# Kernel optimization log

Measured on AMD Instinct MI355X. Metric: run time of the kernel, lower is better.

## Reference

```python
import jax, jax.numpy as jnp
import numpy as np

B, LT, LI, D, H, K = 32, 512, 576, 768, 8, 512


def setup_inputs() -> dict:
    key = jax.random.key(0)
    ks = jax.random.split(key, 10)
    s = 0.02
    return {
        "text_hidden_states": jax.random.normal(ks[0], (B, LT, D), jnp.float32),
        "image_hidden_states": jax.random.normal(ks[1], (B, LI, D), jnp.float32),
        "text_mask": jnp.ones((B, LT), jnp.int32),
        "Wb": jax.random.normal(ks[2], (H, D, D), jnp.float32) * s,   # per-head Linear weights [out,in]
        "Wv": jax.random.normal(ks[3], (K, D), jnp.float32) * s,
        "Wq": jax.random.normal(ks[4], (K, D), jnp.float32) * s,
        "Whv": jax.random.normal(ks[5], (K,), jnp.float32) * s,
        "Whq": jax.random.normal(ks[6], (K,), jnp.float32) * s,
        "Wo": jax.random.normal(ks[7], (D, D * H), jnp.float32) * s,  # output_proj weight [out,in]
        "bo": jnp.zeros((D,), jnp.float32),
    }


def reference(text_hidden_states, image_hidden_states, text_mask, Wb, Wv, Wq, Whv, Whq, Wo, bo):
    text, image = text_hidden_states, image_hidden_states
    # per-head text projection (torch Linear: x @ W.T), batched over heads
    pt = jnp.einsum('bxe,hfe->hbxf', text, Wb)                 # [H,B,LT,D]
    aff = jnp.einsum('hbxe,bye->hbxy', pt, image)              # [H,B,LT,LI]
    wv_v = jnp.einsum('bye,ke->byk', image, Wv)                # [B,LI,K] (head-shared)
    wq_q = jnp.einsum('bxe,ke->bxk', text, Wq)                 # [B,LT,K]
    wqqc = jnp.einsum('bxk,hbxy->hbyk', wq_q, aff)             # [H,B,LI,K]
    wvvc = jnp.einsum('byk,hbxy->hbxk', wv_v, aff)             # [H,B,LT,K]
    h_v = jnp.tanh(wv_v[None] + wqqc)
    h_q = jnp.tanh(wq_q[None] + wvvc)
    att_v = jax.nn.softmax(jnp.einsum('hbyk,k->hby', h_v, Whv), axis=-1)  # over image tokens
    att_q = jax.nn.softmax(jnp.einsum('hbxk,k->hbx', h_q, Whq), axis=-1)  # over text tokens
    ctx_v = jnp.einsum('hby,byd->hbd', att_v, image)
    ctx_q = jnp.einsum('hbx,bxd->hbd', att_q, text)
    head_out = ctx_v + ctx_q                                   # [H,B,D]
    combined = jnp.transpose(head_out, (1, 0, 2)).reshape(text.shape[0], -1)  # [B,H*D]
    return combined @ Wo.T + bo
```

## Files before the change

kernel.cpp:

```cpp
#include <hip/hip_runtime.h>
#include <math.h>

#define B_  32
#define LT_ 512
#define LI_ 576
#define LIP 640
#define D_  768
#define H_  8
#define K_  512
#define NTOK  (LI_ + LT_)
#define CSPLIT 8
#define TPB   (NTOK / CSPLIT)
#define NHEAD ((long)H_ * B_ * D_)

typedef __attribute__((ext_vector_type(4))) short short4v;
typedef __attribute__((ext_vector_type(8))) unsigned short ushort8;
typedef __attribute__((ext_vector_type(8))) _Float16 f16x8;
typedef __attribute__((ext_vector_type(4))) float f32x4;

__device__ __forceinline__ unsigned short f2h(float x) {
  _Float16 h = (_Float16)x;
  return __builtin_bit_cast(unsigned short, h);
}
__device__ __forceinline__ float h2f(unsigned short u) {
  return (float)__builtin_bit_cast(_Float16, u);
}
__device__ __forceinline__ float ftanh(float x) {
  float e = __expf(2.f * x);
  return 1.f - 2.f * __builtin_amdgcn_rcpf(e + 1.f);
}

__device__ __forceinline__ void gl_lds16(const void* g, void* l) {
  __builtin_amdgcn_global_load_lds(
      (const __attribute__((address_space(1))) void*)g,
      (__attribute__((address_space(3))) void*)l, 16, 0, 0);
}

__device__ __forceinline__ f16x8 lds_read16(const unsigned short* p) {
  f16x8 r;
  const __attribute__((address_space(3))) unsigned short* lp =
      (const __attribute__((address_space(3))) unsigned short*)p;
  asm volatile("ds_read_b128 %0, %1" : "=v"(r) : "v"(lp));
  return r;
}

#define EPI_PLAIN 0
#define EPI_T     1
#define EPI_TANH  2
#define EPI_OUT   3

struct Seg {
  const unsigned short *A, *B;
  unsigned short *C, *CT;
  const unsigned short* base;
  const float* wvec;
  float* outv;
  long sA, sB, sC, sCT, sBase;
  int Kd, lda, ldb;
  int gx, gy, nblk, epi, Mlim, valid, ldc, ldt;
};
struct Params { Seg s0, s1, s2; };

__global__ __launch_bounds__(512, 6) void mfma_seg(Params p)
{
  const int orig = blockIdx.x, nwg = gridDim.x;
  const int q8 = nwg >> 3, r8 = nwg & 7;
  const int xcd = orig & 7, idx = orig >> 3;
  const int wg = (xcd < r8 ? xcd * (q8 + 1) : r8 * (q8 + 1) + (xcd - r8) * q8) + idx;

  Seg sg; int local;
  if (wg < p.s0.nblk)                      { sg = p.s0; local = wg; }
  else if (wg < p.s0.nblk + p.s1.nblk)     { sg = p.s1; local = wg - p.s0.nblk; }
  else                                     { sg = p.s2; local = wg - p.s0.nblk - p.s1.nblk; }

  const int bx = local % sg.gx;
  const int tmp2 = local / sg.gx;
  const int by = tmp2 % sg.gy, bz = tmp2 / sg.gy;

  __shared__ unsigned short LDSU[24576];

  const int t = threadIdx.x, lane = t & 63, w = t >> 6;
  const int wr = w >> 2, wc = w & 3;
  const int m0 = bx * 128, n0 = by * 128;
  const int Kd = sg.Kd, lda = sg.lda, ldb = sg.ldb, ldc = sg.ldc;
  const unsigned short* A  = sg.A + (long)bz * sg.sA;
  const unsigned short* Bm = sg.B + (long)bz * sg.sB;

  const int srow = w * 16 + (lane >> 2);
  const int cswz = ((lane & 3) ^ ((srow >> 1) & 3)) * 8;
  const bool clampA = (m0 + 128 > sg.Mlim);
  const unsigned short* aSrc = A  + (long)(m0 + srow) * lda + cswz;
  const unsigned short* bSrc = Bm + (long)(n0 + srow) * ldb + cswz;
  const int ldsLane = w * 512 + lane * 8;

  f32x4 acc[4][2];
  #pragma unroll
  for (int i = 0; i < 4; ++i)
    #pragma unroll
    for (int j = 0; j < 2; ++j)
      acc[i][j] = (f32x4){0.f, 0.f, 0.f, 0.f};

  const int rl = lane & 15, g = lane >> 4;
  const int aslot = (g ^ ((rl >> 1) & 3)) << 3;

  auto stage = [&](int bufi, int k0) {
    unsigned short* Ab = LDSU + bufi * 8192;
    unsigned short* Bb = Ab + 4096;
    if (!clampA) {
      gl_lds16(aSrc + k0, Ab + ldsLane);
    } else {
      int r0 = m0 + srow;
      if (r0 >= sg.Mlim) r0 = sg.Mlim - 1;
      gl_lds16(A + (long)r0 * lda + cswz + k0, Ab + ldsLane);
    }
    gl_lds16(bSrc + k0, Bb + ldsLane);
  };

  const int nt = Kd >> 5;
  stage(0, 0); stage(1, 32); stage(2, 64);
  for (int tt = 0; tt < nt; ++tt) {
    const int ahead = nt - 1 - tt;
    if (ahead >= 2)      asm volatile("s_waitcnt vmcnt(4)" ::: "memory");
    else if (ahead == 1) asm volatile("s_waitcnt vmcnt(2)" ::: "memory");
    else                 asm volatile("s_waitcnt vmcnt(0)" ::: "memory");
    __builtin_amdgcn_s_barrier();

    const unsigned short* Ab = LDSU + (tt % 3) * 8192;
    const unsigned short* Bb = Ab + 4096;
    f16x8 af[4], bf[2];
    #pragma unroll
    for (int i = 0; i < 4; ++i)
      af[i] = lds_read16(&Ab[(wr * 64 + i * 16 + rl) * 32 + aslot]);
    #pragma unroll
    for (int j = 0; j < 2; ++j)
      bf[j] = lds_read16(&Bb[(wc * 32 + j * 16 + rl) * 32 + aslot]);
    asm volatile("s_waitcnt lgkmcnt(0)" ::: "memory");
    __builtin_amdgcn_sched_barrier(0);

    __builtin_amdgcn_s_setprio(1);
    #pragma unroll
    for (int i = 0; i < 4; ++i)
      #pragma unroll
      for (int j = 0; j < 2; ++j)
        acc[i][j] = __builtin_amdgcn_mfma_f32_16x16x32_f16(af[i], bf[j], acc[i][j], 0, 0, 0);
    __builtin_amdgcn_s_setprio(0);

    __builtin_amdgcn_s_barrier();
    if (tt + 3 < nt) stage(tt % 3, (tt + 3) << 5);
  }

  const int rg = lane >> 4;
  if (sg.epi <= EPI_T) {
    unsigned short* C = sg.C + (long)bz * sg.sC;
    unsigned short hv[4][2][4];
    #pragma unroll
    for (int i = 0; i < 4; ++i)
      #pragma unroll
      for (int j = 0; j < 2; ++j)
        #pragma unroll
        for (int rr = 0; rr < 4; ++rr) {
          int ml = wr * 64 + i * 16 + rg * 4 + rr;
          int nl = wc * 32 + j * 16 + rl;
          hv[i][j][rr] = f2h(acc[i][j][rr]);
          if (m0 + ml < sg.Mlim)
            C[(long)(m0 + ml) * ldc + n0 + nl] = hv[i][j][rr];
        }
    if (sg.epi == EPI_T) {
      unsigned short* CT = sg.CT + (long)bz * sg.sCT;
      #pragma unroll
      for (int i = 0; i < 4; ++i)
        #pragma unroll
        for (int j = 0; j < 2; ++j) {
          int nl = wc * 32 + j * 16 + rl;
          int mh = wr * 64 + i * 16 + rg * 4;
          *(short4v*)&LDSU[nl * 136 + mh] = (short4v){
              (short)hv[i][j][0], (short)hv[i][j][1],
              (short)hv[i][j][2], (short)hv[i][j][3]};
        }
      __syncthreads();
      #pragma unroll
      for (int rr = 0; rr < 4; ++rr) {
        int rn = rr * 32 + (t >> 4);
        int m8 = (t & 15) * 8;
        if (m0 + m8 < sg.Mlim)
          *(ushort8*)(CT + (long)(n0 + rn) * sg.ldt + m0 + m8) =
              *(const ushort8*)&LDSU[rn * 136 + m8];
      }
    }
  } else if (sg.epi == EPI_TANH) {
    const unsigned short* base = sg.base + (long)bz * sg.sBase;
    float* outp = sg.outv + (long)bz * sg.valid;
    #pragma unroll
    for (int i = 0; i < 4; ++i)
      #pragma unroll
      for (int rr = 0; rr < 4; ++rr) {
        int row = m0 + wr * 64 + i * 16 + rg * 4 + rr;
        if (row < sg.Mlim) {
          float s = 0.f;
          #pragma unroll
          for (int j = 0; j < 2; ++j) {
            int col = n0 + wc * 32 + j * 16 + rl;
            float v = acc[i][j][rr] + h2f(base[(long)row * ldc + col]);
            s += ftanh(v) * sg.wvec[col];
          }
          s += __shfl_xor(s, 1, 64);
          s += __shfl_xor(s, 2, 64);
          s += __shfl_xor(s, 4, 64);
          s += __shfl_xor(s, 8, 64);
          if (rl == 0 && row < sg.valid)
            atomicAdd(&outp[row], s);
        }
      }
  } else {
    float* outp = sg.outv;
    if (wr == 0) {
      #pragma unroll
      for (int i = 0; i < 2; ++i)
        #pragma unroll
        for (int rr = 0; rr < 4; ++rr) {
          int row = i * 16 + rg * 4 + rr;
          #pragma unroll
          for (int j = 0; j < 2; ++j) {
            int col = n0 + wc * 32 + j * 16 + rl;
            atomicAdd(&outp[(long)row * ldc + col], acc[i][j][rr]);
          }
        }
    }
  }
}

struct CSeg { const float* src; unsigned short* dst; long n8; };

__global__ __launch_bounds__(256) void cast_multi(
    CSeg c0, CSeg c1, CSeg c2, CSeg c3, CSeg c4)
{
  long i = (long)blockIdx.x * 256 + threadIdx.x;
  const float* src; unsigned short* dst;
  if      (i < c0.n8)                 { src = c0.src; dst = c0.dst; }
  else if ((i -= c0.n8) < c1.n8)      { src = c1.src; dst = c1.dst; }
  else if ((i -= c1.n8) < c2.n8)      { src = c2.src; dst = c2.dst; }
  else if ((i -= c2.n8) < c3.n8)      { src = c3.src; dst = c3.dst; }
  else if ((i -= c3.n8) < c4.n8)      { src = c4.src; dst = c4.dst; }
  else return;
  float4 v0 = ((const float4*)src)[i * 2];
  float4 v1 = ((const float4*)src)[i * 2 + 1];
  ushort8 o;
  o[0] = f2h(v0.x); o[1] = f2h(v0.y); o[2] = f2h(v0.z); o[3] = f2h(v0.w);
  o[4] = f2h(v1.x); o[5] = f2h(v1.y); o[6] = f2h(v1.z); o[7] = f2h(v1.w);
  *(ushort8*)(dst + i * 8) = o;
}

__global__ __launch_bounds__(256) void cast_pad_image(
    const float* __restrict__ in, unsigned short* __restrict__ out)
{
  long tid = (long)blockIdx.x * 256 + threadIdx.x;
  const long tot = (long)B_ * LIP * (D_ / 8);
  if (tid >= tot) return;
  int e8 = (int)(tid % (D_ / 8));
  long rw = tid / (D_ / 8);
  int y  = (int)(rw % LIP);
  long b = rw / LIP;
  ushort8 o;
  if (y < LI_) {
    const float* p = in + ((b * LI_ + y) * D_ + e8 * 8);
    float4 v0 = *(const float4*)p, v1 = *(const float4*)(p + 4);
    o[0] = f2h(v0.x); o[1] = f2h(v0.y); o[2] = f2h(v0.z); o[3] = f2h(v0.w);
    o[4] = f2h(v1.x); o[5] = f2h(v1.y); o[6] = f2h(v1.z); o[7] = f2h(v1.w);
  } else {
    #pragma unroll
    for (int j = 0; j < 8; ++j) o[j] = 0;
  }
  *(ushort8*)(out + rw * D_ + e8 * 8) = o;
}

__global__ __launch_bounds__(256) void zero_f32(float* __restrict__ p, long n) {
  long i = (long)blockIdx.x * 256 + threadIdx.x;
  if (i < n) p[i] = 0.f;
}

__global__ __launch_bounds__(256) void init_out(
    const float* __restrict__ bo, float* __restrict__ out)
{
  int i = blockIdx.x * 256 + threadIdx.x;
  out[i] = bo[i % D_];
}

__global__ __launch_bounds__(256) void softmax_att(
    const float* __restrict__ lv, const float* __restrict__ lq,
    float* __restrict__ attvG, float* __restrict__ attqG)
{
  const int b = blockIdx.x, h = blockIdx.y;
  const int t = threadIdx.x;
  __shared__ float buf[LI_];
  __shared__ float red[4];

  const float* lvp = lv + ((long)h * B_ + b) * LI_;
  float m = -1e30f;
  for (int i = t; i < LI_; i += 256) m = fmaxf(m, lvp[i]);
  #pragma unroll
  for (int o = 32; o > 0; o >>= 1) m = fmaxf(m, __shfl_down(m, o, 64));
  if ((t & 63) == 0) red[t >> 6] = m;
  __syncthreads();
  m = fmaxf(fmaxf(red[0], red[1]), fmaxf(red[2], red[3]));
  __syncthreads();
  float s = 0.f;
  for (int i = t; i < LI_; i += 256) { float e = __expf(lvp[i] - m); buf[i] = e; s += e; }
  #pragma unroll
  for (int o = 32; o > 0; o >>= 1) s += __shfl_down(s, o, 64);
  if ((t & 63) == 0) red[t >> 6] = s;
  __syncthreads();
  s = red[0] + red[1] + red[2] + red[3];
  {
    float inv = 1.f / s;
    float* op = attvG + ((long)h * B_ + b) * LI_;
    for (int i = t; i < LI_; i += 256) op[i] = buf[i] * inv;
  }
  __syncthreads();

  const float* lqp = lq + ((long)h * B_ + b) * LT_;
  m = -1e30f;
  for (int i = t; i < LT_; i += 256) m = fmaxf(m, lqp[i]);
  #pragma unroll
  for (int o = 32; o > 0; o >>= 1) m = fmaxf(m, __shfl_down(m, o, 64));
  if ((t & 63) == 0) red[t >> 6] = m;
  __syncthreads();
  m = fmaxf(fmaxf(red[0], red[1]), fmaxf(red[2], red[3]));
  __syncthreads();
  s = 0.f;
  for (int i = t; i < LT_; i += 256) { float e = __expf(lqp[i] - m); buf[i] = e; s += e; }
  #pragma unroll
  for (int o = 32; o > 0; o >>= 1) s += __shfl_down(s, o, 64);
  if ((t & 63) == 0) red[t >> 6] = s;
  __syncthreads();
  s = red[0] + red[1] + red[2] + red[3];
  {
    float inv = 1.f / s;
    float* op = attqG + ((long)h * B_ + b) * LT_;
    for (int i = t; i < LT_; i += 256) op[i] = buf[i] * inv;
  }
}

__global__ __launch_bounds__(256) void ctx_part(
    const float* __restrict__ attvG, const float* __restrict__ attqG,
    const unsigned short* __restrict__ text_h,
    float* __restrict__ head_part)
{
  const int b = blockIdx.x, d0 = blockIdx.y * 128, s = blockIdx.z;
  const int t = threadIdx.x, dl = t & 127, g = t >> 7;
  const long IMG_OFF = (long)B_ * LT_ * D_;
  __shared__ float wts[H_][TPB];
  __shared__ long  roff[TPB];
  __shared__ float red[H_][128];
  const int tok0 = s * TPB;
  for (int i = t; i < H_ * TPB; i += 256) {
    int h = i / TPB, j = i % TPB, tok = tok0 + j;
    wts[h][j] = tok < LI_ ? attvG[((long)h * B_ + b) * LI_ + tok]
                          : attqG[((long)h * B_ + b) * LT_ + (tok - LI_)];
  }
  if (t < TPB) {
    int tok = tok0 + t;
    roff[t] = tok < LI_ ? IMG_OFF + ((long)b * LIP + tok) * D_
                        : ((long)b * LT_ + (tok - LI_)) * D_;
  }
  __syncthreads();
  float acc[H_];
  #pragma unroll
  for (int h = 0; h < H_; ++h) acc[h] = 0.f;
  #pragma unroll 4
  for (int j = g; j < TPB; j += 2) {
    float val = h2f(text_h[roff[j] + d0 + dl]);
    #pragma unroll
    for (int h = 0; h < H_; ++h) acc[h] = fmaf(wts[h][j], val, acc[h]);
  }
  if (g == 1) {
    #pragma unroll
    for (int h = 0; h < H_; ++h) red[h][dl] = acc[h];
  }
  __syncthreads();
  if (g == 0) {
    float* hp = head_part + (long)s * NHEAD;
    #pragma unroll
    for (int h = 0; h < H_; ++h)
      hp[((long)h * B_ + b) * D_ + d0 + dl] = acc[h] + red[h][dl];
  }
}

__global__ __launch_bounds__(256) void reduce_head(
    const float* __restrict__ head_part, unsigned short* __restrict__ head16)
{
  long i = (long)blockIdx.x * 256 + threadIdx.x;
  float s = 0.f;
  #pragma unroll
  for (int p = 0; p < CSPLIT; ++p) s += head_part[(long)p * NHEAD + i];
  int d = (int)(i % D_);
  long hb = i / D_;
  int b = (int)(hb % B_), h = (int)(hb / B_);
  head16[(long)b * (H_ * D_) + (long)h * D_ + d] = f2h(s);
}

extern "C" void kernel_launch(void* const* d_in, const int* in_sizes, int n_in,
                              void* d_out, int out_size, void* d_ws, size_t ws_size,
                              hipStream_t stream)
{
  const float* text  = (const float*)d_in[0];
  const float* image = (const float*)d_in[1];
  const float* Wb  = (const float*)d_in[3];
  const float* Wv  = (const float*)d_in[4];
  const float* Wq  = (const float*)d_in[5];
  const float* Whv = (const float*)d_in[6];
  const float* Whq = (const float*)d_in[7];
  const float* Wo  = (const float*)d_in[8];
  const float* bo  = (const float*)d_in[9];
  float* out = (float*)d_out;

  const long N_TEXT = (long)B_ * LT_ * D_;
  const long N_IMGP = (long)B_ * LIP * D_;
  const long N_WV   = (long)K_ * D_;
  const long N_WB   = (long)H_ * D_ * D_;
  const long N_WO   = (long)D_ * H_ * D_;
  const long N_WVV  = (long)B_ * LIP * K_;
  const long N_WQQ  = (long)B_ * LT_ * K_;
  const long N_PT   = (long)B_ * LT_ * D_;
  const long N_AFF  = (long)B_ * LT_ * LIP;
  const long N_LV   = (long)H_ * B_ * LI_;
  const long N_LQ   = (long)H_ * B_ * LT_;
  const long N_H16  = (long)B_ * H_ * D_;

  unsigned short* wsu = (unsigned short*)d_ws;
  long off = 0;
  unsigned short* text_h  = wsu + off; off += N_TEXT;
  unsigned short* image_p = wsu + off; off += N_IMGP;
  unsigned short* Wv_h    = wsu + off; off += N_WV;
  unsigned short* Wq_h    = wsu + off; off += N_WV;
  unsigned short* Wb_h    = wsu + off; off += N_WB;
  unsigned short* Wo_h    = wsu + off; off += N_WO;
  unsigned short* wv_v    = wsu + off; off += N_WVV;
  unsigned short* wq_q    = wsu + off; off += N_WQQ;
  unsigned short* wv_vT   = wsu + off; off += N_WVV;
  unsigned short* wq_qT   = wsu + off; off += N_WQQ;
  unsigned short* pt_h    = wsu + off; off += N_PT;
  unsigned short* aff     = wsu + off; off += N_AFF;
  unsigned short* affT    = wsu + off; off += N_AFF;
  unsigned short* head16  = wsu + off; off += N_H16;
  float* lv        = (float*)(wsu + off);
  float* lq        = lv + N_LV;
  float* attvG     = lq + N_LQ;
  float* attqG     = attvG + N_LV;
  float* head_part = attqG + N_LQ;
  const size_t need = (size_t)off * 2 +
      (size_t)(2 * (N_LV + N_LQ) + CSPLIT * NHEAD) * 4;
  if (ws_size < need) return;

  dim3 blk(256);
  dim3 blkG(512);

  {
    CSeg c0{text, text_h, N_TEXT / 8};
    CSeg c1{Wv,   Wv_h,   N_WV / 8};
    CSeg c2{Wq,   Wq_h,   N_WV / 8};
    CSeg c3{Wb,   Wb_h,   N_WB / 8};
    CSeg c4{Wo,   Wo_h,   N_WO / 8};
    long tot8 = c0.n8 + c1.n8 + c2.n8 + c3.n8 + c4.n8;
    cast_multi<<<(unsigned)((tot8 + 255) / 256), blk, 0, stream>>>(c0, c1, c2, c3, c4);
  }
  cast_pad_image<<<(unsigned)((B_ * LIP * (D_ / 8) + 255) / 256), blk, 0, stream>>>(image, image_p);
  zero_f32<<<(unsigned)((N_LV + N_LQ + 255) / 256), blk, 0, stream>>>(lv, N_LV + N_LQ);
  init_out<<<(unsigned)(B_ * D_ / 256), blk, 0, stream>>>(bo, out);

  Seg zs{};  zs.nblk = 0;

  {
    Seg s0{}; s0.A = image_p; s0.B = Wv_h; s0.C = wv_v; s0.CT = wv_vT;
    s0.sA = (long)LIP * D_; s0.sC = (long)LIP * K_; s0.sCT = (long)K_ * LIP;
    s0.Kd = D_; s0.lda = D_; s0.ldb = D_;
    s0.gx = 5; s0.gy = 4; s0.nblk = 5 * 4 * B_; s0.epi = EPI_T;
    s0.Mlim = LIP; s0.ldc = K_; s0.ldt = LIP;

    Seg s1{}; s1.A = text_h; s1.B = Wq_h; s1.C = wq_q; s1.CT = wq_qT;
    s1.sA = (long)LT_ * D_; s1.sC = (long)LT_ * K_; s1.sCT = (long)K_ * LT_;
    s1.Kd = D_; s1.lda = D_; s1.ldb = D_;
    s1.gx = 4; s1.gy = 4; s1.nblk = 4 * 4 * B_; s1.epi = EPI_T;
    s1.Mlim = LT_; s1.ldc = K_; s1.ldt = LT_;

    Seg s2{}; s2.A = text_h; s2.B = Wb_h; s2.C = pt_h;
    s2.Kd = D_; s2.lda = D_; s2.ldb = D_;
    s2.gx = 128; s2.gy = 6; s2.nblk = 128 * 6; s2.epi = EPI_PLAIN;
    s2.Mlim = B_ * LT_; s2.ldc = D_;

    Params P{s0, s1, s2};
    mfma_seg<<<s0.nblk + s1.nblk + s2.nblk, blkG, 0, stream>>>(P);
  }

  for (int h = 0; h < H_; ++h) {
    {
      Seg s0{}; s0.A = pt_h; s0.B = image_p; s0.C = aff; s0.CT = affT;
      s0.sA = (long)LT_ * D_; s0.sB = (long)LIP * D_;
      s0.sC = (long)LT_ * LIP; s0.sCT = (long)LIP * LT_;
      s0.Kd = D_; s0.lda = D_; s0.ldb = D_;
      s0.gx = 4; s0.gy = 5; s0.nblk = 4 * 5 * B_; s0.epi = EPI_T;
      s0.Mlim = LT_; s0.ldc = LIP; s0.ldt = LT_;
      Params P{s0, zs, zs};
      mfma_seg<<<s0.nblk, blkG, 0, stream>>>(P);
    }
    {
      Seg s0{}; s0.A = affT; s0.B = wq_qT;
      s0.base = wv_v; s0.wvec = Whv; s0.outv = lv + (long)h * B_ * LI_;
      s0.sA = (long)LIP * LT_; s0.sB = (long)K_ * LT_; s0.sBase = (long)LIP * K_;
      s0.Kd = LT_; s0.lda = LT_; s0.ldb = LT_;
      s0.gx = 5; s0.gy = 4; s0.nblk = 5 * 4 * B_; s0.epi = EPI_TANH;
      s0.Mlim = LIP; s0.valid = LI_; s0.ldc = K_;

      Seg s1{}; s1.A = aff; s1.B = wv_vT;
      s1.base = wq_q; s1.wvec = Whq; s1.outv = lq + (long)h * B_ * LT_;
      s1.sA = (long)LT_ * LIP; s1.sB = (long)K_ * LIP; s1.sBase = (long)LT_ * K_;
      s1.Kd = LIP; s1.lda = LIP; s1.ldb = LIP;
      s1.gx = 4; s1.gy = 4; s1.nblk = 4 * 4 * B_; s1.epi = EPI_TANH;
      s1.Mlim = LT_; s1.valid = LT_; s1.ldc = K_;

      Seg s2 = zs;
      if (h < H_ - 1) {
        s2.A = text_h; s2.B = Wb_h + (long)(h + 1) * D_ * D_; s2.C = pt_h;
        s2.Kd = D_; s2.lda = D_; s2.ldb = D_;
        s2.gx = 128; s2.gy = 6; s2.nblk = 128 * 6; s2.epi = EPI_PLAIN;
        s2.Mlim = B_ * LT_; s2.ldc = D_;
      }
      Params P{s0, s1, s2};
      mfma_seg<<<s0.nblk + s1.nblk + s2.nblk, blkG, 0, stream>>>(P);
    }
  }

  softmax_att<<<dim3(B_, H_), blk, 0, stream>>>(lv, lq, attvG, attqG);
  ctx_part<<<dim3(B_, D_ / 128, CSPLIT), blk, 0, stream>>>(attvG, attqG, text_h, head_part);
  reduce_head<<<(unsigned)(NHEAD / 256), blk, 0, stream>>>(head_part, head16);

  {
    Seg s0{}; s0.A = head16; s0.B = Wo_h; s0.outv = out;
    s0.sA = (long)(H_ * D_ / 8); s0.sB = (long)(H_ * D_ / 8);
    s0.Kd = H_ * D_ / 8; s0.lda = H_ * D_; s0.ldb = H_ * D_;
    s0.gx = 1; s0.gy = 6; s0.nblk = 1 * 6 * 8; s0.epi = EPI_OUT;
    s0.Mlim = B_; s0.valid = B_; s0.ldc = D_;
    Params P{s0, zs, zs};
    mfma_seg<<<s0.nblk, blkG, 0, stream>>>(P);
  }
}
```

Before: 997.3 us.

## Replace LDS-staged GEMM mainloop with direct global loads and smaller tiles

The shared MFMA GEMM kernel drops its triple-buffered global-to-LDS staging with barriers. Each wave now loads its A/B fragments directly from global memory into registers, double-buffered across k-steps. Block tiles shrink from 128x128 with 512 threads to 128x64 with 256 threads, and every launch's grid doubles in N to match. This removes the LDS traffic and barrier synchronisation, but it loses LDS-based data sharing between waves, so global and L2 traffic rise and rows are read without the swizzled coalescing.

```diff
diff --git a/kernel.cpp b/kernel.cpp
--- a/kernel.cpp
+++ b/kernel.cpp
@@ -30,20 +30,6 @@
   return 1.f - 2.f * __builtin_amdgcn_rcpf(e + 1.f);
 }
 
-__device__ __forceinline__ void gl_lds16(const void* g, void* l) {
-  __builtin_amdgcn_global_load_lds(
-      (const __attribute__((address_space(1))) void*)g,
-      (__attribute__((address_space(3))) void*)l, 16, 0, 0);
-}
-
-__device__ __forceinline__ f16x8 lds_read16(const unsigned short* p) {
-  f16x8 r;
-  const __attribute__((address_space(3))) unsigned short* lp =
-      (const __attribute__((address_space(3))) unsigned short*)p;
-  asm volatile("ds_read_b128 %0, %1" : "=v"(r) : "v"(lp));
-  return r;
-}
-
 #define EPI_PLAIN 0
 #define EPI_T     1
 #define EPI_TANH  2
@@ -61,7 +47,7 @@
 };
 struct Params { Seg s0, s1, s2; };
 
-__global__ __launch_bounds__(512, 6) void mfma_seg(Params p)
+__global__ __launch_bounds__(256, 4) void mfma_seg(Params p)
 {
   const int orig = blockIdx.x, nwg = gridDim.x;
   const int q8 = nwg >> 3, r8 = nwg & 7;
@@ -77,21 +63,31 @@
   const int tmp2 = local / sg.gx;
   const int by = tmp2 % sg.gy, bz = tmp2 / sg.gy;
 
-  __shared__ unsigned short LDSU[24576];
+  __shared__ unsigned short LDSU[64 * 136];
 
   const int t = threadIdx.x, lane = t & 63, w = t >> 6;
-  const int wr = w >> 2, wc = w & 3;
-  const int m0 = bx * 128, n0 = by * 128;
+  const int wr = w >> 1, wc = w & 1;
+  const int m0 = bx * 128, n0 = by * 64;
   const int Kd = sg.Kd, lda = sg.lda, ldb = sg.ldb, ldc = sg.ldc;
   const unsigned short* A  = sg.A + (long)bz * sg.sA;
   const unsigned short* Bm = sg.B + (long)bz * sg.sB;
 
-  const int srow = w * 16 + (lane >> 2);
-  const int cswz = ((lane & 3) ^ ((srow >> 1) & 3)) * 8;
-  const bool clampA = (m0 + 128 > sg.Mlim);
-  const unsigned short* aSrc = A  + (long)(m0 + srow) * lda + cswz;
-  const unsigned short* bSrc = Bm + (long)(n0 + srow) * ldb + cswz;
-  const int ldsLane = w * 512 + lane * 8;
+  const int rl = lane & 15, g = lane >> 4;
+
+  const unsigned short* aP0; const unsigned short* aP1;
+  const unsigned short* aP2; const unsigned short* aP3;
+  {
+    int r0 = m0 + wr * 64 + 0  + rl;  if (r0 >= sg.Mlim) r0 = sg.Mlim - 1;
+    int r1 = m0 + wr * 64 + 16 + rl;  if (r1 >= sg.Mlim) r1 = sg.Mlim - 1;
+    int r2 = m0 + wr * 64 + 32 + rl;  if (r2 >= sg.Mlim) r2 = sg.Mlim - 1;
+    int r3 = m0 + wr * 64 + 48 + rl;  if (r3 >= sg.Mlim) r3 = sg.Mlim - 1;
+    aP0 = A + (long)r0 * lda + g * 8;
+    aP1 = A + (long)r1 * lda + g * 8;
+    aP2 = A + (long)r2 * lda + g * 8;
+    aP3 = A + (long)r3 * lda + g * 8;
+  }
+  const unsigned short* bP0 = Bm + (long)(n0 + wc * 32 + 0  + rl) * ldb + g * 8;
+  const unsigned short* bP1 = Bm + (long)(n0 + wc * 32 + 16 + rl) * ldb + g * 8;
 
   f32x4 acc[4][2];
   #pragma unroll
@@ -100,53 +96,35 @@
     for (int j = 0; j < 2; ++j)
       acc[i][j] = (f32x4){0.f, 0.f, 0.f, 0.f};
 
-  const int rl = lane & 15, g = lane >> 4;
-  const int aslot = (g ^ ((rl >> 1) & 3)) << 3;
-
-  auto stage = [&](int bufi, int k0) {
-    unsigned short* Ab = LDSU + bufi * 8192;
-    unsigned short* Bb = Ab + 4096;
-    if (!clampA) {
-      gl_lds16(aSrc + k0, Ab + ldsLane);
-    } else {
-      int r0 = m0 + srow;
-      if (r0 >= sg.Mlim) r0 = sg.Mlim - 1;
-      gl_lds16(A + (long)r0 * lda + cswz + k0, Ab + ldsLane);
-    }
-    gl_lds16(bSrc + k0, Bb + ldsLane);
-  };
+  f16x8 a0_0, a0_1, a0_2, a0_3, b0_0, b0_1;
+  f16x8 a1_0, a1_1, a1_2, a1_3, b1_0, b1_1;
+
+#define LOADSET(s, kk)                                        \
+  { int koff = (kk);                                          \
+    a##s##_0 = *(const f16x8*)(aP0 + koff);                   \
+    a##s##_1 = *(const f16x8*)(aP1 + koff);                   \
+    a##s##_2 = *(const f16x8*)(aP2 + koff);                   \
+    a##s##_3 = *(const f16x8*)(aP3 + koff);                   \
+    b##s##_0 = *(const f16x8*)(bP0 + koff);                   \
+    b##s##_1 = *(const f16x8*)(bP1 + koff); }
+
+#define MMASET(s)                                                             \
+  { acc[0][0] = __builtin_amdgcn_mfma_f32_16x16x32_f16(a##s##_0, b##s##_0, acc[0][0], 0, 0, 0); \
+    acc[0][1] = __builtin_amdgcn_mfma_f32_16x16x32_f16(a##s##_0, b##s##_1, acc[0][1], 0, 0, 0); \
+    acc[1][0] = __builtin_amdgcn_mfma_f32_16x16x32_f16(a##s##_1, b##s##_0, acc[1][0], 0, 0, 0); \
+    acc[1][1] = __builtin_amdgcn_mfma_f32_16x16x32_f16(a##s##_1, b##s##_1, acc[1][1], 0, 0, 0); \
+    acc[2][0] = __builtin_amdgcn_mfma_f32_16x16x32_f16(a##s##_2, b##s##_0, acc[2][0], 0, 0, 0); \
+    acc[2][1] = __builtin_amdgcn_mfma_f32_16x16x32_f16(a##s##_2, b##s##_1, acc[2][1], 0, 0, 0); \
+    acc[3][0] = __builtin_amdgcn_mfma_f32_16x16x32_f16(a##s##_3, b##s##_0, acc[3][0], 0, 0, 0); \
+    acc[3][1] = __builtin_amdgcn_mfma_f32_16x16x32_f16(a##s##_3, b##s##_1, acc[3][1], 0, 0, 0); }
 
   const int nt = Kd >> 5;
-  stage(0, 0); stage(1, 32); stage(2, 64);
-  for (int tt = 0; tt < nt; ++tt) {
-    const int ahead = nt - 1 - tt;
-    if (ahead >= 2)      asm volatile("s_waitcnt vmcnt(4)" ::: "memory");
-    else if (ahead == 1) asm volatile("s_waitcnt vmcnt(2)" ::: "memory");
-    else                 asm volatile("s_waitcnt vmcnt(0)" ::: "memory");
-    __builtin_amdgcn_s_barrier();
-
-    const unsigned short* Ab = LDSU + (tt % 3) * 8192;
-    const unsigned short* Bb = Ab + 4096;
-    f16x8 af[4], bf[2];
-    #pragma unroll
-    for (int i = 0; i < 4; ++i)
-      af[i] = lds_read16(&Ab[(wr * 64 + i * 16 + rl) * 32 + aslot]);
-    #pragma unroll
-    for (int j = 0; j < 2; ++j)
-      bf[j] = lds_read16(&Bb[(wc * 32 + j * 16 + rl) * 32 + aslot]);
-    asm volatile("s_waitcnt lgkmcnt(0)" ::: "memory");
-    __builtin_amdgcn_sched_barrier(0);
-
-    __builtin_amdgcn_s_setprio(1);
-    #pragma unroll
-    for (int i = 0; i < 4; ++i)
-      #pragma unroll
-      for (int j = 0; j < 2; ++j)
-        acc[i][j] = __builtin_amdgcn_mfma_f32_16x16x32_f16(af[i], bf[j], acc[i][j], 0, 0, 0);
-    __builtin_amdgcn_s_setprio(0);
-
-    __builtin_amdgcn_s_barrier();
-    if (tt + 3 < nt) stage(tt % 3, (tt + 3) << 5);
+  LOADSET(0, 0)
+  for (int tt = 0; tt < nt; tt += 2) {
+    if (tt + 1 < nt) LOADSET(1, (tt + 1) * 32)
+    MMASET(0)
+    if (tt + 2 < nt) LOADSET(0, (tt + 2) * 32)
+    MMASET(1)
   }
 
   const int rg = lane >> 4;
@@ -180,7 +158,7 @@
       __syncthreads();
       #pragma unroll
       for (int rr = 0; rr < 4; ++rr) {
-        int rn = rr * 32 + (t >> 4);
+        int rn = rr * 16 + (t >> 4);
         int m8 = (t & 15) * 8;
         if (m0 + m8 < sg.Mlim)
           *(ushort8*)(CT + (long)(n0 + rn) * sg.ldt + m0 + m8) =
@@ -227,6 +205,8 @@
         }
     }
   }
+#undef LOADSET
+#undef MMASET
 }
 
 struct CSeg { const float* src; unsigned short* dst; long n8; };
@@ -452,7 +432,6 @@
   if (ws_size < need) return;
 
   dim3 blk(256);
-  dim3 blkG(512);
 
   {
     CSeg c0{text, text_h, N_TEXT / 8};
@@ -473,22 +452,22 @@
     Seg s0{}; s0.A = image_p; s0.B = Wv_h; s0.C = wv_v; s0.CT = wv_vT;
     s0.sA = (long)LIP * D_; s0.sC = (long)LIP * K_; s0.sCT = (long)K_ * LIP;
     s0.Kd = D_; s0.lda = D_; s0.ldb = D_;
-    s0.gx = 5; s0.gy = 4; s0.nblk = 5 * 4 * B_; s0.epi = EPI_T;
+    s0.gx = 5; s0.gy = 8; s0.nblk = 5 * 8 * B_; s0.epi = EPI_T;
     s0.Mlim = LIP; s0.ldc = K_; s0.ldt = LIP;
 
     Seg s1{}; s1.A = text_h; s1.B = Wq_h; s1.C = wq_q; s1.CT = wq_qT;
     s1.sA = (long)LT_ * D_; s1.sC = (long)LT_ * K_; s1.sCT = (long)K_ * LT_;
     s1.Kd = D_; s1.lda = D_; s1.ldb = D_;
-    s1.gx = 4; s1.gy = 4; s1.nblk = 4 * 4 * B_; s1.epi = EPI_T;
+    s1.gx = 4; s1.gy = 8; s1.nblk = 4 * 8 * B_; s1.epi = EPI_T;
     s1.Mlim = LT_; s1.ldc = K_; s1.ldt = LT_;
 
     Seg s2{}; s2.A = text_h; s2.B = Wb_h; s2.C = pt_h;
     s2.Kd = D_; s2.lda = D_; s2.ldb = D_;
-    s2.gx = 128; s2.gy = 6; s2.nblk = 128 * 6; s2.epi = EPI_PLAIN;
+    s2.gx = 128; s2.gy = 12; s2.nblk = 128 * 12; s2.epi = EPI_PLAIN;
     s2.Mlim = B_ * LT_; s2.ldc = D_;
 
     Params P{s0, s1, s2};
-    mfma_seg<<<s0.nblk + s1.nblk + s2.nblk, blkG, 0, stream>>>(P);
+    mfma_seg<<<s0.nblk + s1.nblk + s2.nblk, blk, 0, stream>>>(P);
   }
 
   for (int h = 0; h < H_; ++h) {
@@ -497,35 +476,35 @@
       s0.sA = (long)LT_ * D_; s0.sB = (long)LIP * D_;
       s0.sC = (long)LT_ * LIP; s0.sCT = (long)LIP * LT_;
       s0.Kd = D_; s0.lda = D_; s0.ldb = D_;
-      s0.gx = 4; s0.gy = 5; s0.nblk = 4 * 5 * B_; s0.epi = EPI_T;
+      s0.gx = 4; s0.gy = 10; s0.nblk = 4 * 10 * B_; s0.epi = EPI_T;
       s0.Mlim = LT_; s0.ldc = LIP; s0.ldt = LT_;
       Params P{s0, zs, zs};
-      mfma_seg<<<s0.nblk, blkG, 0, stream>>>(P);
+      mfma_seg<<<s0.nblk, blk, 0, stream>>>(P);
     }
     {
       Seg s0{}; s0.A = affT; s0.B = wq_qT;
       s0.base = wv_v; s0.wvec = Whv; s0.outv = lv + (long)h * B_ * LI_;
       s0.sA = (long)LIP * LT_; s0.sB = (long)K_ * LT_; s0.sBase = (long)LIP * K_;
       s0.Kd = LT_; s0.lda = LT_; s0.ldb = LT_;
-      s0.gx = 5; s0.gy = 4; s0.nblk = 5 * 4 * B_; s0.epi = EPI_TANH;
+      s0.gx = 5; s0.gy = 8; s0.nblk = 5 * 8 * B_; s0.epi = EPI_TANH;
       s0.Mlim = LIP; s0.valid = LI_; s0.ldc = K_;
 
       Seg s1{}; s1.A = aff; s1.B = wv_vT;
       s1.base = wq_q; s1.wvec = Whq; s1.outv = lq + (long)h * B_ * LT_;
       s1.sA = (long)LT_ * LIP; s1.sB = (long)K_ * LIP; s1.sBase = (long)LT_ * K_;
       s1.Kd = LIP; s1.lda = LIP; s1.ldb = LIP;
-      s1.gx = 4; s1.gy = 4; s1.nblk = 4 * 4 * B_; s1.epi = EPI_TANH;
+      s1.gx = 4; s1.gy = 8; s1.nblk = 4 * 8 * B_; s1.epi = EPI_TANH;
       s1.Mlim = LT_; s1.valid = LT_; s1.ldc = K_;
 
       Seg s2 = zs;
       if (h < H_ - 1) {
         s2.A = text_h; s2.B = Wb_h + (long)(h + 1) * D_ * D_; s2.C = pt_h;
         s2.Kd = D_; s2.lda = D_; s2.ldb = D_;
-        s2.gx = 128; s2.gy = 6; s2.nblk = 128 * 6; s2.epi = EPI_PLAIN;
+        s2.gx = 128; s2.gy = 12; s2.nblk = 128 * 12; s2.epi = EPI_PLAIN;
         s2.Mlim = B_ * LT_; s2.ldc = D_;
       }
       Params P{s0, s1, s2};
-      mfma_seg<<<s0.nblk + s1.nblk + s2.nblk, blkG, 0, stream>>>(P);
+      mfma_seg<<<s0.nblk + s1.nblk + s2.nblk, blk, 0, stream>>>(P);
     }
   }
 
@@ -537,9 +516,9 @@
     Seg s0{}; s0.A = head16; s0.B = Wo_h; s0.outv = out;
     s0.sA = (long)(H_ * D_ / 8); s0.sB = (long)(H_ * D_ / 8);
     s0.Kd = H_ * D_ / 8; s0.lda = H_ * D_; s0.ldb = H_ * D_;
-    s0.gx = 1; s0.gy = 6; s0.nblk = 1 * 6 * 8; s0.epi = EPI_OUT;
+    s0.gx = 1; s0.gy = 12; s0.nblk = 1 * 12 * 8; s0.epi = EPI_OUT;
     s0.Mlim = B_; s0.valid = B_; s0.ldc = D_;
     Params P{s0, zs, zs};
-    mfma_seg<<<s0.nblk, blkG, 0, stream>>>(P);
-  }
-}
+    mfma_seg<<<s0.nblk, blk, 0, stream>>>(P);
+  }
+}
```

After: 2.845 ms. +185.3%, slower.
